# Optimization experiments

Hardware: AMD Instinct MI355X
Metric: run time of the kernel (lower is better)

The kernel has to match this reference:

```python
import jax, jax.numpy as jnp
import numpy as np

N = 50000
E = 800000
IN_DIM = 128
HID = 128
ENC_DIM = 128
TASK_DIM = 64


def setup_inputs() -> dict:
    key = jax.random.key(0)
    ks = jax.random.split(key, 8)
    x = jax.random.normal(ks[0], (N, IN_DIM), dtype=jnp.float32)
    edge_index = jax.random.randint(ks[1], (2, E), 0, N, dtype=jnp.int64)
    s1 = 1.0 / np.sqrt(IN_DIM)
    s2 = 1.0 / np.sqrt(HID)
    W1 = jax.random.uniform(ks[2], (IN_DIM, HID), jnp.float32, -s1, s1)
    b1 = jnp.zeros((HID,), jnp.float32)
    W2 = jax.random.uniform(ks[3], (HID, ENC_DIM), jnp.float32, -s2, s2)
    b2 = jnp.zeros((ENC_DIM,), jnp.float32)
    sh = 1.0 / np.sqrt(ENC_DIM)
    Wh = jax.random.uniform(ks[4], (ENC_DIM, TASK_DIM), jnp.float32, -sh, sh)
    bh = jax.random.uniform(ks[5], (TASK_DIM,), jnp.float32, -sh, sh)
    return {"x": x, "edge_index": edge_index, "W1": W1, "b1": b1,
            "W2": W2, "b2": b2, "Wh": Wh, "bh": bh}


def _gcn_conv(x, src, dst, norm, W, b):
    # GCNConv: linear transform, then normalized sum-aggregation over edges
    h = x @ W                                   # [N, D_out]
    msg = h[src] * norm[:, None]                # [E', D_out] gather
    agg = jax.ops.segment_sum(msg, dst, num_segments=N)  # scatter-add
    return agg + b


def reference(x, edge_index, W1, b1, W2, b2, Wh, bh):
    src, dst = edge_index[0], edge_index[1]
    # add self-loops (standard GCN)
    loops = jnp.arange(N, dtype=src.dtype)
    src = jnp.concatenate([src, loops])
    dst = jnp.concatenate([dst, loops])
    # symmetric normalization: deg^{-1/2}[src] * deg^{-1/2}[dst]
    ones = jnp.ones_like(dst, dtype=x.dtype)
    deg = jax.ops.segment_sum(ones, dst, num_segments=N)
    dinv = jnp.where(deg > 0, jax.lax.rsqrt(deg), 0.0)
    norm = dinv[src] * dinv[dst]                # [E']

    h = _gcn_conv(x, src, dst, norm, W1, b1)
    h = jax.nn.relu(h)
    h = _gcn_conv(h, src, dst, norm, W2, b2)
    # per-task linear head
    return h @ Wh + bh
```

## Files before the change

### kernel.cpp

```cpp
#include <hip/hip_runtime.h>


typedef _Float16 half8 __attribute__((ext_vector_type(8)));
typedef _Float16 half2v __attribute__((ext_vector_type(2)));
typedef float f32x4 __attribute__((ext_vector_type(4)));
typedef unsigned short ushort8v __attribute__((ext_vector_type(8)));
typedef unsigned short ushort4v __attribute__((ext_vector_type(4)));

constexpr int DIM = 128;
constexpr int CAP = 64;
constexpr int BCAP = 5120;

__global__ __launch_bounds__(256) void k_prep(
    const float* __restrict__ W1, const float* __restrict__ W2,
    const float* __restrict__ Wh, const float* __restrict__ b2,
    const float* __restrict__ bh, float* __restrict__ W2h,
    float* __restrict__ bconst, _Float16* __restrict__ W1p,
    int* __restrict__ cursor, int nb) {
    int b = blockIdx.x, t = threadIdx.x;
    if (b < 32) {
        int gid = b * 256 + t;
        int r = gid >> 6, c = gid & 63;
        float s = 0.f;
        for (int k = 0; k < 128; ++k) s += W2[r * 128 + k] * Wh[k * 64 + c];
        W2h[gid] = s;
    } else if (b == 32) {
        if (t < 64) {
            float s = bh[t];
            for (int k = 0; k < 128; ++k) s += b2[k] * Wh[k * 64 + t];
            bconst[t] = s;
        }
        if (t < nb) cursor[t] = 0;
    } else {
        int q = (b - 33) * 256 + t;
        int lane = q & 63, ct = (q >> 6) & 7, ks = q >> 9;
        int kb = 32 * ks + 8 * (lane >> 4);
        int col = 16 * ct + (lane & 15);
        half8 v;
#pragma unroll
        for (int i = 0; i < 8; ++i) v[i] = (_Float16)W1[(kb + i) * 128 + col];
        *(half8*)&W1p[(size_t)q * 8] = v;
    }
}

__global__ __launch_bounds__(256) void k_bucket(
    const int* __restrict__ src, const int* __restrict__ dst,
    int* __restrict__ cursor, unsigned int* __restrict__ pairs,
    const float* __restrict__ W2h, _Float16* __restrict__ W2p, int e) {
    if (blockIdx.x == gridDim.x - 1) {
        int q0 = threadIdx.x * 4;
#pragma unroll
        for (int j = 0; j < 4; ++j) {
            int q = q0 + j;
            int lane = q & 63, ct = (q >> 6) & 3, ks = q >> 8;
            int kb = 32 * ks + 8 * (lane >> 4);
            int col = 16 * ct + (lane & 15);
            half8 v;
#pragma unroll
            for (int i = 0; i < 8; ++i) v[i] = (_Float16)W2h[(kb + i) * 64 + col];
            *(half8*)&W2p[(size_t)q * 8] = v;
        }
        return;
    }
    __shared__ int lcnt[256];
    __shared__ int lbase[256];
    int tid = threadIdx.x;
    int base = blockIdx.x * 4096;
    int endi = min(base + 4096, e);

    for (int i = tid; i < 256; i += 256) lcnt[i] = 0;
    __syncthreads();

    for (int i = base + tid * 4; i < endi; i += 1024) {
        if (i + 3 < endi) {
            int4 d4 = *(const int4*)(dst + i);
            atomicAdd(&lcnt[d4.x >> 8], 1);
            atomicAdd(&lcnt[d4.y >> 8], 1);
            atomicAdd(&lcnt[d4.z >> 8], 1);
            atomicAdd(&lcnt[d4.w >> 8], 1);
        } else {
            for (int k = i; k < endi; ++k) atomicAdd(&lcnt[dst[k] >> 8], 1);
        }
    }
    __syncthreads();

    if (tid < 256) {
        int c = lcnt[tid];
        lbase[tid] = (c > 0) ? atomicAdd(&cursor[tid], c) : 0;
    }
    __syncthreads();
    for (int i = tid; i < 256; i += 256) lcnt[i] = 0;
    __syncthreads();

    for (int i = base + tid * 4; i < endi; i += 1024) {
        if (i + 3 < endi) {
            int4 d4 = *(const int4*)(dst + i);
            int4 s4 = *(const int4*)(src + i);
            {
                int bk = d4.x >> 8;
                int gi = lbase[bk] + atomicAdd(&lcnt[bk], 1);
                if (gi < BCAP) pairs[(size_t)bk * BCAP + gi] =
                    (unsigned)s4.x | ((unsigned)(d4.x & 255) << 16);
            }
            {
                int bk = d4.y >> 8;
                int gi = lbase[bk] + atomicAdd(&lcnt[bk], 1);
                if (gi < BCAP) pairs[(size_t)bk * BCAP + gi] =
                    (unsigned)s4.y | ((unsigned)(d4.y & 255) << 16);
            }
            {
                int bk = d4.z >> 8;
                int gi = lbase[bk] + atomicAdd(&lcnt[bk], 1);
                if (gi < BCAP) pairs[(size_t)bk * BCAP + gi] =
                    (unsigned)s4.z | ((unsigned)(d4.z & 255) << 16);
            }
            {
                int bk = d4.w >> 8;
                int gi = lbase[bk] + atomicAdd(&lcnt[bk], 1);
                if (gi < BCAP) pairs[(size_t)bk * BCAP + gi] =
                    (unsigned)s4.w | ((unsigned)(d4.w & 255) << 16);
            }
        } else {
            for (int k = i; k < endi; ++k) {
                int d = dst[k];
                int bk = d >> 8;
                int gi = lbase[bk] + atomicAdd(&lcnt[bk], 1);
                if (gi < BCAP) pairs[(size_t)bk * BCAP + gi] =
                    (unsigned)src[k] | ((unsigned)(d & 255) << 16);
            }
        }
    }
}

__global__ __launch_bounds__(256) void k_bins(
    const unsigned int* __restrict__ pairs, const int* __restrict__ cursor,
    unsigned short* __restrict__ csr, int* __restrict__ cnt,
    float* __restrict__ dinv, int n) {
    __shared__ int lcnt[256];
    int bkt = blockIdx.x;
    int tid = threadIdx.x;
    lcnt[tid] = 0;
    __syncthreads();
    int total = min(cursor[bkt], BCAP);
    const unsigned int* run = pairs + (size_t)bkt * BCAP;
    int nbase = bkt << 8;
    for (int i = tid; i < total; i += 256) {
        unsigned p = run[i];
        int dloc = p >> 16;
        int pos = atomicAdd(&lcnt[dloc], 1);
        if (pos < CAP)
            csr[(size_t)(nbase + dloc) * CAP + pos] = (unsigned short)(p & 0xFFFF);
    }
    __syncthreads();
    int node = nbase + tid;
    if (node < n) {
        int c = min(lcnt[tid], CAP);
        cnt[node] = c;
        dinv[node] = rsqrtf((float)(lcnt[tid] + 1));
    }
}

template <int NCOL, bool AF16>
__global__ __launch_bounds__(256) void k_gemm(
    const void* __restrict__ Asrc, const _Float16* __restrict__ Bp,
    const float* __restrict__ rscale, _Float16* __restrict__ Cout, int n) {
    constexpr int CT = NCOL / 16;
    constexpr int BCHUNK = 4 * CT * 64;
    __shared__ _Float16 Bs[BCHUNK * 8];
    __shared__ _Float16 As[8192];

    int tid = threadIdx.x;
    int row0 = blockIdx.x * 64;

    {
        const uint4* sp = (const uint4*)Bp;
        uint4* dp = (uint4*)Bs;
        for (int i = tid; i < BCHUNK; i += 256) dp[i] = sp[i];
    }
    for (int q = tid; q < 1024; q += 256) {
        int l = q & 63, s = q >> 6;
        int w = s >> 2, ks = s & 3;
        int row = row0 + 16 * w + (l & 15);
        int k0 = 32 * ks + 8 * (l >> 4);
        half8 v;
#pragma unroll
        for (int i = 0; i < 8; ++i) v[i] = (_Float16)0.f;
        if (row < n) {
            if constexpr (AF16) {
                v = *(const half8*)((const _Float16*)Asrc + (size_t)row * 128 + k0);
            } else {
                const float* p = (const float*)Asrc + (size_t)row * 128 + k0;
                f32x4 lo = *(const f32x4*)p;
                f32x4 hi = *(const f32x4*)(p + 4);
                v[0] = (_Float16)lo[0]; v[1] = (_Float16)lo[1];
                v[2] = (_Float16)lo[2]; v[3] = (_Float16)lo[3];
                v[4] = (_Float16)hi[0]; v[5] = (_Float16)hi[1];
                v[6] = (_Float16)hi[2]; v[7] = (_Float16)hi[3];
            }
        }
        *(half8*)&As[(size_t)q * 8] = v;
    }
    __syncthreads();

    int w = tid >> 6, lane = tid & 63;
    f32x4 acc[CT];
#pragma unroll
    for (int ct = 0; ct < CT; ++ct) acc[ct] = (f32x4){0.f, 0.f, 0.f, 0.f};
#pragma unroll
    for (int ks = 0; ks < 4; ++ks) {
        half8 a = *(const half8*)&As[((w * 4 + ks) * 64 + lane) * 8];
#pragma unroll
        for (int ct = 0; ct < CT; ++ct) {
            half8 b = *(const half8*)&Bs[((ks * CT + ct) * 64 + lane) * 8];
            acc[ct] = __builtin_amdgcn_mfma_f32_16x16x32_f16(a, b, acc[ct], 0, 0, 0);
        }
    }
    __syncthreads();

    int rg = lane >> 4, cl = lane & 15;
    float sc[4];
#pragma unroll
    for (int r = 0; r < 4; ++r) {
        int row = row0 + 16 * w + 4 * rg + r;
        sc[r] = (row < n) ? rscale[row] : 0.f;
    }
#pragma unroll
    for (int ct = 0; ct < CT; ++ct)
#pragma unroll
        for (int r = 0; r < 4; ++r)
            As[(16 * w + 4 * rg + r) * NCOL + 16 * ct + cl] =
                (_Float16)(acc[ct][r] * sc[r]);
    __syncthreads();

    constexpr int CHROW = NCOL / 8;
    for (int c = tid; c < 64 * CHROW; c += 256) {
        int r = c / CHROW;
        int row = row0 + r;
        if (row < n)
            *(half8*)(Cout + (size_t)row * NCOL + (size_t)(c - r * CHROW) * 8) =
                *(const half8*)&As[c * 8];
    }
}

__global__ __launch_bounds__(256) void k_gather_l1(
    const int* __restrict__ cnt, const float* __restrict__ dinv,
    const unsigned short* __restrict__ csr, const _Float16* __restrict__ hs,
    const float* __restrict__ b1, _Float16* __restrict__ hA, int n) {
    int g = (blockIdx.x * 256 + threadIdx.x) >> 6;
    int lane = threadIdx.x & 63;
    if (g >= n) return;
    const half2v* h2 = (const half2v*)hs;
    int deg = cnt[g];
    float dg = dinv[g];
    half2v hv = h2[(size_t)g * 64 + lane];
    float a0 = (float)hv[0], a1 = (float)hv[1];
    float c0 = 0.f, c1 = 0.f;
    const unsigned short* row = csr + (size_t)g * CAP;
    int j = 0;
    for (; j + 8 <= deg; j += 8) {
        ushort8v s8 = *(const ushort8v*)(row + j);
        half2v v0 = h2[(size_t)s8[0] * 64 + lane];
        half2v v1 = h2[(size_t)s8[1] * 64 + lane];
        half2v v2 = h2[(size_t)s8[2] * 64 + lane];
        half2v v3 = h2[(size_t)s8[3] * 64 + lane];
        half2v v4 = h2[(size_t)s8[4] * 64 + lane];
        half2v v5 = h2[(size_t)s8[5] * 64 + lane];
        half2v v6 = h2[(size_t)s8[6] * 64 + lane];
        half2v v7 = h2[(size_t)s8[7] * 64 + lane];
        a0 += (float)v0[0]; a1 += (float)v0[1];
        c0 += (float)v1[0]; c1 += (float)v1[1];
        a0 += (float)v2[0]; a1 += (float)v2[1];
        c0 += (float)v3[0]; c1 += (float)v3[1];
        a0 += (float)v4[0]; a1 += (float)v4[1];
        c0 += (float)v5[0]; c1 += (float)v5[1];
        a0 += (float)v6[0]; a1 += (float)v6[1];
        c0 += (float)v7[0]; c1 += (float)v7[1];
    }
    if (j + 4 <= deg) {
        ushort4v s4 = *(const ushort4v*)(row + j);
        half2v v0 = h2[(size_t)s4[0] * 64 + lane];
        half2v v1 = h2[(size_t)s4[1] * 64 + lane];
        half2v v2 = h2[(size_t)s4[2] * 64 + lane];
        half2v v3 = h2[(size_t)s4[3] * 64 + lane];
        a0 += (float)v0[0]; a1 += (float)v0[1];
        c0 += (float)v1[0]; c1 += (float)v1[1];
        a0 += (float)v2[0]; a1 += (float)v2[1];
        c0 += (float)v3[0]; c1 += (float)v3[1];
        j += 4;
    }
    for (; j < deg; ++j) {
        half2v v0 = h2[(size_t)row[j] * 64 + lane];
        a0 += (float)v0[0]; a1 += (float)v0[1];
    }
    float2 bb = *(const float2*)(b1 + lane * 2);
    half2v o;
    o[0] = (_Float16)fmaxf((a0 + c0) * dg + bb.x, 0.f);
    o[1] = (_Float16)fmaxf((a1 + c1) * dg + bb.y, 0.f);
    *(half2v*)(hA + (size_t)g * 128 + lane * 2) = o;
}

__global__ __launch_bounds__(256) void k_gather_l2(
    const int* __restrict__ cnt, const float* __restrict__ dinv,
    const unsigned short* __restrict__ csr, const _Float16* __restrict__ hs,
    const float* __restrict__ bconst, float* __restrict__ outp, int n) {
    int g = (blockIdx.x * 256 + threadIdx.x) >> 5;
    int lane = threadIdx.x & 31;
    if (g >= n) return;
    const half2v* hp = (const half2v*)hs;
    int deg = cnt[g];
    float dg = dinv[g];
    half2v hv = hp[(size_t)g * 32 + lane];
    float a0 = (float)hv[0], a1 = (float)hv[1];
    float c0 = 0.f, c1 = 0.f;
    const unsigned short* row = csr + (size_t)g * CAP;
    int j = 0;
    for (; j + 8 <= deg; j += 8) {
        ushort8v s8 = *(const ushort8v*)(row + j);
        half2v v0 = hp[(size_t)s8[0] * 32 + lane];
        half2v v1 = hp[(size_t)s8[1] * 32 + lane];
        half2v v2 = hp[(size_t)s8[2] * 32 + lane];
        half2v v3 = hp[(size_t)s8[3] * 32 + lane];
        half2v v4 = hp[(size_t)s8[4] * 32 + lane];
        half2v v5 = hp[(size_t)s8[5] * 32 + lane];
        half2v v6 = hp[(size_t)s8[6] * 32 + lane];
        half2v v7 = hp[(size_t)s8[7] * 32 + lane];
        a0 += (float)v0[0]; a1 += (float)v0[1];
        c0 += (float)v1[0]; c1 += (float)v1[1];
        a0 += (float)v2[0]; a1 += (float)v2[1];
        c0 += (float)v3[0]; c1 += (float)v3[1];
        a0 += (float)v4[0]; a1 += (float)v4[1];
        c0 += (float)v5[0]; c1 += (float)v5[1];
        a0 += (float)v6[0]; a1 += (float)v6[1];
        c0 += (float)v7[0]; c1 += (float)v7[1];
    }
    if (j + 4 <= deg) {
        ushort4v s4 = *(const ushort4v*)(row + j);
        half2v v0 = hp[(size_t)s4[0] * 32 + lane];
        half2v v1 = hp[(size_t)s4[1] * 32 + lane];
        half2v v2 = hp[(size_t)s4[2] * 32 + lane];
        half2v v3 = hp[(size_t)s4[3] * 32 + lane];
        a0 += (float)v0[0]; a1 += (float)v0[1];
        c0 += (float)v1[0]; c1 += (float)v1[1];
        a0 += (float)v2[0]; a1 += (float)v2[1];
        c0 += (float)v3[0]; c1 += (float)v3[1];
        j += 4;
    }
    for (; j < deg; ++j) {
        half2v v0 = hp[(size_t)row[j] * 32 + lane];
        a0 += (float)v0[0]; a1 += (float)v0[1];
    }
    float2 bc = *(const float2*)(bconst + lane * 2);
    *(float2*)(outp + (size_t)g * 64 + lane * 2) =
        make_float2((a0 + c0) * dg + bc.x, (a1 + c1) * dg + bc.y);
}

extern "C" void kernel_launch(void* const* d_in, const int* in_sizes, int n_in,
                              void* d_out, int out_size, void* d_ws, size_t ws_size,
                              hipStream_t stream) {
    const float* x  = (const float*)d_in[0];
    const int*   ei = (const int*)d_in[1];
    const float* W1 = (const float*)d_in[2];
    const float* b1 = (const float*)d_in[3];
    const float* W2 = (const float*)d_in[4];
    const float* b2 = (const float*)d_in[5];
    const float* Wh = (const float*)d_in[6];
    const float* bh = (const float*)d_in[7];
    float* out = (float*)d_out;

    const int n = in_sizes[0] / DIM;
    const int e = in_sizes[1] / 2;
    const int* src = ei;
    const int* dst = ei + e;
    const int nb = (n + 255) >> 8;

    char* wsp = (char*)d_ws;
    auto alloc = [&](size_t bytes) {
        char* p = wsp;
        wsp += (bytes + 255) & ~(size_t)255;
        return p;
    };
    int*            cnt    = (int*)alloc((size_t)n * 4);
    float*          dinv   = (float*)alloc((size_t)n * 4);
    float*          W2h    = (float*)alloc(8192 * 4);
    float*          bconst = (float*)alloc(64 * 4);
    _Float16*       W1p    = (_Float16*)alloc(16384 * 2);
    _Float16*       W2p    = (_Float16*)alloc(8192 * 2);
    int*            cursor = (int*)alloc((size_t)nb * 4);
    unsigned int*   pairs  = (unsigned int*)alloc((size_t)nb * BCAP * 4);
    unsigned short* csr    = (unsigned short*)alloc((size_t)n * CAP * 2);
    _Float16*       hbuf   = (_Float16*)alloc((size_t)n * 128 * 2);
    _Float16*       hA     = (_Float16*)alloc((size_t)n * 128 * 2);
    _Float16*       h2     = (_Float16*)alloc((size_t)n * 64 * 2);

    int gbGemm = (n + 63) / 64;
    int gbBkt  = (e + 4095) / 4096 + 1;
    int gbW64  = (int)(((size_t)n * 64 + 255) / 256);
    int gbW32  = (int)(((size_t)n * 32 + 255) / 256);

    k_prep<<<41, 256, 0, stream>>>(W1, W2, Wh, b2, bh, W2h, bconst, W1p,
                                   cursor, nb);
    k_bucket<<<gbBkt, 256, 0, stream>>>(src, dst, cursor, pairs, W2h, W2p, e);
    k_bins<<<nb, 256, 0, stream>>>(pairs, cursor, csr, cnt, dinv, n);

    k_gemm<128, false><<<gbGemm, 256, 0, stream>>>((const void*)x, W1p, dinv, hbuf, n);
    k_gather_l1<<<gbW64, 256, 0, stream>>>(cnt, dinv, csr, hbuf, b1, hA, n);
    k_gemm<64, true><<<gbGemm, 256, 0, stream>>>((const void*)hA, W2p, dinv, h2, n);
    k_gather_l2<<<gbW32, 256, 0, stream>>>(cnt, dinv, csr, h2, bconst, out, n);
}
```

Measured before the change: 104.4 us.

## Replace global bucket cursors with per-chunk local scan and merge prep kernel

Bucketing now writes each edge chunk's pairs locally, sorted by destination bucket using a shared-memory prefix scan. Per-chunk counts and offsets go to global arrays instead of using global atomic cursors with a fixed per-bucket capacity. The bins kernel has each thread walk one chunk's run for its bucket. The weight-prep work is folded into the bucket and bins launches, which removes one kernel launch and the cursor zeroing. The cost is that each bins thread reads short, scattered runs, about 196 runs per bucket done serially by the first threads, so load balance in bins may get worse.

After: 103.1 us. No clear change (-1.2%).

```diff
diff --git a/kernel.cpp b/kernel.cpp
--- a/kernel.cpp
+++ b/kernel.cpp
@@ -9,66 +9,50 @@
 
 constexpr int DIM = 128;
 constexpr int CAP = 64;
-constexpr int BCAP = 5120;
-
-__global__ __launch_bounds__(256) void k_prep(
+constexpr int ECHUNK = 4096;
+
+__global__ __launch_bounds__(256) void k_bucket(
+    const int* __restrict__ src, const int* __restrict__ dst,
     const float* __restrict__ W1, const float* __restrict__ W2,
     const float* __restrict__ Wh, const float* __restrict__ b2,
     const float* __restrict__ bh, float* __restrict__ W2h,
     float* __restrict__ bconst, _Float16* __restrict__ W1p,
-    int* __restrict__ cursor, int nb) {
-    int b = blockIdx.x, t = threadIdx.x;
-    if (b < 32) {
-        int gid = b * 256 + t;
-        int r = gid >> 6, c = gid & 63;
-        float s = 0.f;
-        for (int k = 0; k < 128; ++k) s += W2[r * 128 + k] * Wh[k * 64 + c];
-        W2h[gid] = s;
-    } else if (b == 32) {
-        if (t < 64) {
-            float s = bh[t];
-            for (int k = 0; k < 128; ++k) s += b2[k] * Wh[k * 64 + t];
-            bconst[t] = s;
-        }
-        if (t < nb) cursor[t] = 0;
-    } else {
-        int q = (b - 33) * 256 + t;
-        int lane = q & 63, ct = (q >> 6) & 7, ks = q >> 9;
-        int kb = 32 * ks + 8 * (lane >> 4);
-        int col = 16 * ct + (lane & 15);
-        half8 v;
-#pragma unroll
-        for (int i = 0; i < 8; ++i) v[i] = (_Float16)W1[(kb + i) * 128 + col];
-        *(half8*)&W1p[(size_t)q * 8] = v;
-    }
-}
-
-__global__ __launch_bounds__(256) void k_bucket(
-    const int* __restrict__ src, const int* __restrict__ dst,
-    int* __restrict__ cursor, unsigned int* __restrict__ pairs,
-    const float* __restrict__ W2h, _Float16* __restrict__ W2p, int e) {
-    if (blockIdx.x == gridDim.x - 1) {
-        int q0 = threadIdx.x * 4;
-#pragma unroll
-        for (int j = 0; j < 4; ++j) {
-            int q = q0 + j;
-            int lane = q & 63, ct = (q >> 6) & 3, ks = q >> 8;
+    int* __restrict__ bcnt, int* __restrict__ boff,
+    unsigned int* __restrict__ pairs, int e, int nchunk) {
+    int tid = threadIdx.x;
+    if (blockIdx.x >= nchunk) {
+        int pb = blockIdx.x - nchunk;
+        if (pb < 32) {
+            int gid = pb * 256 + tid;
+            int r = gid >> 6, c = gid & 63;
+            float s = 0.f;
+            for (int k = 0; k < 128; ++k) s += W2[r * 128 + k] * Wh[k * 64 + c];
+            W2h[gid] = s;
+        } else if (pb == 32) {
+            if (tid < 64) {
+                float s = bh[tid];
+                for (int k = 0; k < 128; ++k) s += b2[k] * Wh[k * 64 + tid];
+                bconst[tid] = s;
+            }
+        } else {
+            int q = (pb - 33) * 256 + tid;
+            int lane = q & 63, ct = (q >> 6) & 7, ks = q >> 9;
             int kb = 32 * ks + 8 * (lane >> 4);
             int col = 16 * ct + (lane & 15);
             half8 v;
 #pragma unroll
-            for (int i = 0; i < 8; ++i) v[i] = (_Float16)W2h[(kb + i) * 64 + col];
-            *(half8*)&W2p[(size_t)q * 8] = v;
+            for (int i = 0; i < 8; ++i) v[i] = (_Float16)W1[(kb + i) * 128 + col];
+            *(half8*)&W1p[(size_t)q * 8] = v;
         }
         return;
     }
     __shared__ int lcnt[256];
     __shared__ int lbase[256];
-    int tid = threadIdx.x;
-    int base = blockIdx.x * 4096;
-    int endi = min(base + 4096, e);
-
-    for (int i = tid; i < 256; i += 256) lcnt[i] = 0;
+    int c = blockIdx.x;
+    int base = c * ECHUNK;
+    int endi = min(base + ECHUNK, e);
+
+    lcnt[tid] = 0;
     __syncthreads();
 
     for (int i = base + tid * 4; i < endi; i += 1024) {
@@ -84,12 +68,21 @@
     }
     __syncthreads();
 
-    if (tid < 256) {
-        int c = lcnt[tid];
-        lbase[tid] = (c > 0) ? atomicAdd(&cursor[tid], c) : 0;
-    }
-    __syncthreads();
-    for (int i = tid; i < 256; i += 256) lcnt[i] = 0;
+    int v = lcnt[tid];
+    lbase[tid] = v;
+    __syncthreads();
+    for (int o = 1; o < 256; o <<= 1) {
+        int y = (tid >= o) ? lbase[tid - o] : 0;
+        __syncthreads();
+        lbase[tid] += y;
+        __syncthreads();
+    }
+    int excl = lbase[tid] - v;
+    bcnt[c * 256 + tid] = v;
+    boff[c * 256 + tid] = excl;
+    __syncthreads();
+    lbase[tid] = excl;
+    lcnt[tid] = 0;
     __syncthreads();
 
     for (int i = base + tid * 4; i < endi; i += 1024) {
@@ -99,25 +92,25 @@
             {
                 int bk = d4.x >> 8;
                 int gi = lbase[bk] + atomicAdd(&lcnt[bk], 1);
-                if (gi < BCAP) pairs[(size_t)bk * BCAP + gi] =
+                pairs[(size_t)base + gi] =
                     (unsigned)s4.x | ((unsigned)(d4.x & 255) << 16);
             }
             {
                 int bk = d4.y >> 8;
                 int gi = lbase[bk] + atomicAdd(&lcnt[bk], 1);
-                if (gi < BCAP) pairs[(size_t)bk * BCAP + gi] =
+                pairs[(size_t)base + gi] =
                     (unsigned)s4.y | ((unsigned)(d4.y & 255) << 16);
             }
             {
                 int bk = d4.z >> 8;
                 int gi = lbase[bk] + atomicAdd(&lcnt[bk], 1);
-                if (gi < BCAP) pairs[(size_t)bk * BCAP + gi] =
+                pairs[(size_t)base + gi] =
                     (unsigned)s4.z | ((unsigned)(d4.z & 255) << 16);
             }
             {
                 int bk = d4.w >> 8;
                 int gi = lbase[bk] + atomicAdd(&lcnt[bk], 1);
-                if (gi < BCAP) pairs[(size_t)bk * BCAP + gi] =
+                pairs[(size_t)base + gi] =
                     (unsigned)s4.w | ((unsigned)(d4.w & 255) << 16);
             }
         } else {
@@ -125,7 +118,7 @@
                 int d = dst[k];
                 int bk = d >> 8;
                 int gi = lbase[bk] + atomicAdd(&lcnt[bk], 1);
-                if (gi < BCAP) pairs[(size_t)bk * BCAP + gi] =
+                pairs[(size_t)base + gi] =
                     (unsigned)src[k] | ((unsigned)(d & 255) << 16);
             }
         }
@@ -133,23 +126,44 @@
 }
 
 __global__ __launch_bounds__(256) void k_bins(
-    const unsigned int* __restrict__ pairs, const int* __restrict__ cursor,
-    unsigned short* __restrict__ csr, int* __restrict__ cnt,
-    float* __restrict__ dinv, int n) {
+    const unsigned int* __restrict__ pairs, const int* __restrict__ bcnt,
+    const int* __restrict__ boff, unsigned short* __restrict__ csr,
+    int* __restrict__ cnt, float* __restrict__ dinv,
+    const float* __restrict__ W2h, _Float16* __restrict__ W2p,
+    int n, int nchunk) {
+    int tid = threadIdx.x;
+    if (blockIdx.x == gridDim.x - 1) {
+        int q0 = tid * 4;
+#pragma unroll
+        for (int j = 0; j < 4; ++j) {
+            int q = q0 + j;
+            int lane = q & 63, ct = (q >> 6) & 3, ks = q >> 8;
+            int kb = 32 * ks + 8 * (lane >> 4);
+            int col = 16 * ct + (lane & 15);
+            half8 v;
+#pragma unroll
+            for (int i = 0; i < 8; ++i) v[i] = (_Float16)W2h[(kb + i) * 64 + col];
+            *(half8*)&W2p[(size_t)q * 8] = v;
+        }
+        return;
+    }
     __shared__ int lcnt[256];
-    int bkt = blockIdx.x;
-    int tid = threadIdx.x;
+    int b = blockIdx.x;
     lcnt[tid] = 0;
     __syncthreads();
-    int total = min(cursor[bkt], BCAP);
-    const unsigned int* run = pairs + (size_t)bkt * BCAP;
-    int nbase = bkt << 8;
-    for (int i = tid; i < total; i += 256) {
-        unsigned p = run[i];
-        int dloc = p >> 16;
-        int pos = atomicAdd(&lcnt[dloc], 1);
-        if (pos < CAP)
-            csr[(size_t)(nbase + dloc) * CAP + pos] = (unsigned short)(p & 0xFFFF);
+    int nbase = b << 8;
+    for (int c = tid; c < nchunk; c += 256) {
+        int len = bcnt[c * 256 + b];
+        int off = boff[c * 256 + b];
+        const unsigned int* run = pairs + (size_t)c * ECHUNK + off;
+        for (int i = 0; i < len; ++i) {
+            unsigned p = run[i];
+            int dloc = p >> 16;
+            int pos = atomicAdd(&lcnt[dloc], 1);
+            if (pos < CAP)
+                csr[(size_t)(nbase + dloc) * CAP + pos] =
+                    (unsigned short)(p & 0xFFFF);
+        }
     }
     __syncthreads();
     int node = nbase + tid;
@@ -372,6 +386,7 @@
     const int* src = ei;
     const int* dst = ei + e;
     const int nb = (n + 255) >> 8;
+    const int nchunk = (e + ECHUNK - 1) / ECHUNK;
 
     char* wsp = (char*)d_ws;
     auto alloc = [&](size_t bytes) {
@@ -385,22 +400,23 @@
     float*          bconst = (float*)alloc(64 * 4);
     _Float16*       W1p    = (_Float16*)alloc(16384 * 2);
     _Float16*       W2p    = (_Float16*)alloc(8192 * 2);
-    int*            cursor = (int*)alloc((size_t)nb * 4);
-    unsigned int*   pairs  = (unsigned int*)alloc((size_t)nb * BCAP * 4);
+    int*            bcnt   = (int*)alloc((size_t)nchunk * 256 * 4);
+    int*            boff   = (int*)alloc((size_t)nchunk * 256 * 4);
+    unsigned int*   pairs  = (unsigned int*)alloc((size_t)nchunk * ECHUNK * 4);
     unsigned short* csr    = (unsigned short*)alloc((size_t)n * CAP * 2);
     _Float16*       hbuf   = (_Float16*)alloc((size_t)n * 128 * 2);
     _Float16*       hA     = (_Float16*)alloc((size_t)n * 128 * 2);
     _Float16*       h2     = (_Float16*)alloc((size_t)n * 64 * 2);
 
     int gbGemm = (n + 63) / 64;
-    int gbBkt  = (e + 4095) / 4096 + 1;
     int gbW64  = (int)(((size_t)n * 64 + 255) / 256);
     int gbW32  = (int)(((size_t)n * 32 + 255) / 256);
 
-    k_prep<<<41, 256, 0, stream>>>(W1, W2, Wh, b2, bh, W2h, bconst, W1p,
-                                   cursor, nb);
-    k_bucket<<<gbBkt, 256, 0, stream>>>(src, dst, cursor, pairs, W2h, W2p, e);
-    k_bins<<<nb, 256, 0, stream>>>(pairs, cursor, csr, cnt, dinv, n);
+    k_bucket<<<nchunk + 41, 256, 0, stream>>>(
+        src, dst, W1, W2, Wh, b2, bh, W2h, bconst, W1p, bcnt, boff, pairs,
+        e, nchunk);
+    k_bins<<<nb + 1, 256, 0, stream>>>(pairs, bcnt, boff, csr, cnt, dinv,
+                                       W2h, W2p, n, nchunk);
 
     k_gemm<128, false><<<gbGemm, 256, 0, stream>>>((const void*)x, W1p, dinv, hbuf, n);
     k_gather_l1<<<gbW64, 256, 0, stream>>>(cnt, dinv, csr, hbuf, b1, hA, n);
```
